# Optimization experiments

Measured on AMD Instinct MI355X. Metric: run time of the kernel, lower is better.

Reference implementation:

```python
import jax, jax.numpy as jnp
import numpy as np

N_NODES = 100000
IN_F, HID_F, OUT_F = 128, 128, 64
N_EDGES = 1600000


def _gcn_conv(x, src, dst, n, W, b):
    # x: [N, Fin]; src/dst: [E'] (self-loops already appended)
    h = x @ W                                        # [N, Fout]
    deg = jax.ops.segment_sum(jnp.ones_like(dst, dtype=h.dtype), dst,
                              num_segments=n)        # in-degree incl. self-loop
    dinv = jnp.where(deg > 0, jax.lax.rsqrt(deg), 0.0)
    norm = dinv[src] * dinv[dst]                     # [E']
    msg = h[src] * norm[:, None]                     # [E', Fout] gather + scale
    out = jax.ops.segment_sum(msg, dst, num_segments=n)
    return out + b


def setup_inputs() -> dict:
    key = jax.random.key(0)
    ks = jax.random.split(key, 6)
    x = jax.random.normal(ks[0], (N_NODES, IN_F), dtype=jnp.float32)
    edge_index = jax.random.randint(ks[1], (2, N_EDGES), 0, N_NODES, dtype=jnp.int64)
    # Glorot-ish init for weights, zeros for biases (PyG GCNConv default)
    W1 = jax.random.normal(ks[2], (IN_F, HID_F), dtype=jnp.float32) / np.sqrt(IN_F)
    b1 = jnp.zeros((HID_F,), dtype=jnp.float32)
    W2 = jax.random.normal(ks[3], (HID_F, OUT_F), dtype=jnp.float32) / np.sqrt(HID_F)
    b2 = jnp.zeros((OUT_F,), dtype=jnp.float32)
    return {"x": x, "edge_index": edge_index, "W1": W1, "b1": b1, "W2": W2, "b2": b2}


def reference(x, edge_index, W1, b1, W2, b2):
    n = x.shape[0]
    # GCNConv adds self-loops, then symmetric deg^-1/2 normalization
    loops = jnp.arange(n, dtype=edge_index.dtype)
    src = jnp.concatenate([edge_index[0], loops])
    dst = jnp.concatenate([edge_index[1], loops])
    h = _gcn_conv(x, src, dst, n, W1, b1)
    h = jax.nn.relu(h)
    out = _gcn_conv(h, src, dst, n, W2, b2)
    return out
```

## Files before the change

kernel.cpp:

```cpp
#include <hip/hip_runtime.h>
#include <hip/hip_fp16.h>

#define N_NODES 100000
#define N_EDGES 1600000
#define BNODES  128
#define NBUCK   782
#define CAP     3072
#define BIN_TILE 8192
#define BIN_BLOCKS 196
#define LDSK    136


typedef _Float16 half8 __attribute__((ext_vector_type(8)));
typedef float    f32x4 __attribute__((ext_vector_type(4)));

__device__ __forceinline__ float bcf(float v, int l) {
    return __int_as_float(__builtin_amdgcn_readlane(__float_as_int(v), l));
}
__device__ __forceinline__ int bci(int v, int l) {
    return __builtin_amdgcn_readlane(v, l);
}


__global__ __launch_bounds__(1024, 1) void k_bin(const int* __restrict__ src,
                                                 const int* __restrict__ dst,
                                                 int* __restrict__ cursor,
                                                 unsigned int* __restrict__ staged) {
    __shared__ unsigned int stg[BIN_TILE];
    __shared__ unsigned short stgb[BIN_TILE];
    __shared__ int hist[NBUCK];
    __shared__ int lbase[NBUCK];
    __shared__ int gbs[NBUCK];
    __shared__ int wsum[16];

    int t = threadIdx.x;
    int lane = t & 63, wv = t >> 6;
    long base = (long)blockIdx.x * BIN_TILE;
    int nval = (int)min((long)BIN_TILE, (long)N_EDGES - base);

    for (int i = t; i < NBUCK; i += 1024) hist[i] = 0;
    __syncthreads();

    unsigned int ent[8], brk[8];
#pragma unroll
    for (int r = 0; r < 8; r++) {
        int i = r * 1024 + t;
        if (i < nval) {
            int s = src[base + i], d = dst[base + i];
            int b = d >> 7;
            int rk = atomicAdd(&hist[b], 1);
            ent[r] = ((unsigned int)(d & 127) << 17) | (unsigned int)s;
            brk[r] = ((unsigned int)b << 16) | (unsigned int)rk;
        } else {
            brk[r] = 0xFFFFFFFFu;
        }
    }
    __syncthreads();

    {
        int v = (t < NBUCK) ? hist[t] : 0;
        int x = v;
#pragma unroll
        for (int o = 1; o < 64; o <<= 1) {
            int u = __shfl_up(x, o);
            if (lane >= o) x += u;
        }
        if (lane == 63) wsum[wv] = x;
        __syncthreads();
        if (wv == 0) {
            int ws = (lane < 16) ? wsum[lane] : 0;
#pragma unroll
            for (int o = 1; o < 16; o <<= 1) {
                int u = __shfl_up(ws, o);
                if (lane >= o) ws += u;
            }
            if (lane < 16) wsum[lane] = ws;
        }
        __syncthreads();
        int incl = x + (wv > 0 ? wsum[wv - 1] : 0);
        if (t < NBUCK) lbase[t] = incl - v;
    }
    __syncthreads();

#pragma unroll
    for (int r = 0; r < 8; r++) {
        if (brk[r] != 0xFFFFFFFFu) {
            int b  = (int)(brk[r] >> 16);
            int rk = (int)(brk[r] & 0xFFFF);
            int p  = lbase[b] + rk;
            stg[p]  = ent[r];
            stgb[p] = (unsigned short)b;
        }
    }
    __syncthreads();

    if (t < NBUCK) gbs[t] = (hist[t] > 0) ? atomicAdd(&cursor[t], hist[t]) : 0;
    __syncthreads();

    for (int i = t; i < nval; i += 1024) {
        int b = stgb[i];
        int pos = gbs[b] + (i - lbase[b]);
        if (pos < CAP) staged[(size_t)b * CAP + pos] = stg[i];
    }
}


__global__ __launch_bounds__(512) void k_fill3(const unsigned int* __restrict__ staged,
                                               const int* __restrict__ cursor,
                                               int* __restrict__ col,
                                               int2* __restrict__ rpse,
                                               float* __restrict__ dinv) {
    __shared__ int stg[CAP];
    __shared__ int lcnt[BNODES];
    __shared__ int lbase[BNODES];
    __shared__ int lpos[BNODES];
    __shared__ int sscan[BNODES];

    int b = blockIdx.x, t = threadIdx.x;
    int n = min(cursor[b], CAP);
    const unsigned int* sp = staged + (size_t)b * CAP;

    if (t < BNODES) lcnt[t] = 0;
    __syncthreads();

    unsigned int ent[CAP / 512];
#pragma unroll
    for (int r = 0; r < CAP / 512; r++) {
        int i = r * 512 + t;
        if (i < n) {
            ent[r] = sp[i];
            atomicAdd(&lcnt[ent[r] >> 17], 1);
        }
    }
    __syncthreads();

    if (t < BNODES) sscan[t] = lcnt[t];
    __syncthreads();
    for (int o = 1; o < BNODES; o <<= 1) {
        int u = (t < BNODES && t >= o) ? sscan[t - o] : 0;
        __syncthreads();
        if (t < BNODES) sscan[t] += u;
        __syncthreads();
    }
    if (t < BNODES) {
        int ex = sscan[t] - lcnt[t];
        lbase[t] = ex;
        lpos[t]  = ex;
        int node = b * BNODES + t;
        if (node < N_NODES) {
            dinv[node] = rsqrtf((float)(lcnt[t] + 1));
            rpse[node] = make_int2(b * CAP + ex, b * CAP + ex + lcnt[t]);
        }
    }
    __syncthreads();

#pragma unroll
    for (int r = 0; r < CAP / 512; r++) {
        int i = r * 512 + t;
        if (i < n) {
            int dl = (int)(ent[r] >> 17);
            int pos = atomicAdd(&lpos[dl], 1);
            stg[pos] = (int)(ent[r] & 0x1FFFFu);
        }
    }
    __syncthreads();

    for (int i = t; i < n; i += 512) col[(size_t)b * CAP + i] = stg[i];
}


template <int NOUT, bool F32IN>
__global__ __launch_bounds__(256) void k_gemm_mfma(const void* __restrict__ Xv,
                                                   const float* __restrict__ W,
                                                   __half* __restrict__ H) {
    __shared__ _Float16 wt[NOUT * LDSK];
    for (int idx = threadIdx.x; idx < 64 * NOUT; idx += 256) {
        int kp = idx / NOUT;
        int n  = idx - kp * NOUT;
        __half2 p = __floats2half2_rn(W[(2 * kp) * NOUT + n], W[(2 * kp + 1) * NOUT + n]);
        *reinterpret_cast<__half2*>(&wt[n * LDSK + 2 * kp]) = p;
    }
    __syncthreads();

    int wv = threadIdx.x >> 6, l = threadIdx.x & 63;
    int m = l & 15, g = l >> 4;
    int row0 = blockIdx.x * 64 + wv * 16;
    int lrow = min(row0 + m, N_NODES - 1);

    f32x4 acc[NOUT / 16];
#pragma unroll
    for (int c = 0; c < NOUT / 16; c++) acc[c] = (f32x4){0.f, 0.f, 0.f, 0.f};

#pragma unroll
    for (int kk = 0; kk < 4; kk++) {
        int k0 = kk * 32 + g * 8;
        half8 a;
        if (F32IN) {
            const float* xp = (const float*)Xv + (size_t)lrow * 128 + k0;
#pragma unroll
            for (int j = 0; j < 8; j++) a[j] = (_Float16)xp[j];
        } else {
            a = *reinterpret_cast<const half8*>((const _Float16*)Xv + (size_t)lrow * 128 + k0);
        }
#pragma unroll
        for (int c = 0; c < NOUT / 16; c++) {
            half8 b = *reinterpret_cast<const half8*>(&wt[(c * 16 + m) * LDSK + k0]);
            acc[c] = __builtin_amdgcn_mfma_f32_16x16x32_f16(a, b, acc[c], 0, 0, 0);
        }
    }

#pragma unroll
    for (int c = 0; c < NOUT / 16; c++)
#pragma unroll
        for (int r = 0; r < 4; r++) {
            int grow = row0 + g * 4 + r;
            if (grow < N_NODES)
                H[(size_t)grow * NOUT + c * 16 + m] = __float2half(acc[c][r]);
        }
}


__global__ __launch_bounds__(256) void k_agg1(const __half2* __restrict__ H1,
                                              const float* __restrict__ dinv,
                                              const int2* __restrict__ rpse,
                                              const int* __restrict__ col,
                                              const float* __restrict__ b1,
                                              __half2* __restrict__ H2) {
    int node = blockIdx.x * 4 + (threadIdx.x >> 6);
    int lane = threadIdx.x & 63;

    float di = dinv[node];
    int2 se = rpse[node];
    int e0 = se.x, e1 = se.y;

    float2 sv = __half22float2(H1[(size_t)node * 64 + lane]);
    float a0 = sv.x * di * di, a1 = sv.y * di * di;

    for (int cb = e0; cb < e1; cb += 64) {
        int n = min(64, e1 - cb);
        int idx = cb + lane;
        int cv = col[idx < e1 ? idx : e0];
        float wf = dinv[cv] * di;

        int j = 0;
        for (; j + 8 <= n; j += 8) {
            float2 v[8];
            float  w[8];
#pragma unroll
            for (int q = 0; q < 8; q++) {
                int s = bci(cv, j + q);
                w[q] = bcf(wf, j + q);
                v[q] = __half22float2(H1[(size_t)s * 64 + lane]);
            }
#pragma unroll
            for (int q = 0; q < 8; q++) { a0 += v[q].x * w[q]; a1 += v[q].y * w[q]; }
        }
        for (; j < n; j++) {
            int s = bci(cv, j);
            float w = bcf(wf, j);
            float2 v = __half22float2(H1[(size_t)s * 64 + lane]);
            a0 += v.x * w;
            a1 += v.y * w;
        }
    }

    a0 = fmaxf(a0 + b1[2 * lane], 0.f);
    a1 = fmaxf(a1 + b1[2 * lane + 1], 0.f);
    H2[(size_t)node * 64 + lane] = __floats2half2_rn(a0, a1);
}


__global__ __launch_bounds__(256) void k_agg2(const __half* __restrict__ H3,
                                              const float* __restrict__ dinv,
                                              const int2* __restrict__ rpse,
                                              const int* __restrict__ col,
                                              const float* __restrict__ b2,
                                              float* __restrict__ out) {
    int node = (blockIdx.x * 256 + threadIdx.x) >> 6;
    int lane = threadIdx.x & 63;
    if (node >= N_NODES) return;

    float di = dinv[node];
    int2 se = rpse[node];
    int e0 = se.x, e1 = se.y;

    float a = __half2float(H3[(size_t)node * 64 + lane]) * di * di;

    for (int cb = e0; cb < e1; cb += 64) {
        int n = min(64, e1 - cb);
        int idx = cb + lane;
        int cv = col[idx < e1 ? idx : e0];
        float wf = dinv[cv] * di;

        int j = 0;
        for (; j + 8 <= n; j += 8) {
            float hv[8];
            float w[8];
#pragma unroll
            for (int q = 0; q < 8; q++) {
                int s = bci(cv, j + q);
                w[q] = bcf(wf, j + q);
                hv[q] = __half2float(H3[(size_t)s * 64 + lane]);
            }
#pragma unroll
            for (int q = 0; q < 8; q++) a += hv[q] * w[q];
        }
        for (; j < n; j++) {
            int s = bci(cv, j);
            float w = bcf(wf, j);
            a += __half2float(H3[(size_t)s * 64 + lane]) * w;
        }
    }

    out[(size_t)node * 64 + lane] = a + b2[lane];
}


extern "C" void kernel_launch(void* const* d_in, const int* in_sizes, int n_in,
                              void* d_out, int out_size, void* d_ws, size_t ws_size,
                              hipStream_t stream) {
    const float* x  = (const float*)d_in[0];
    const int*   ei = (const int*)d_in[1];
    const float* W1 = (const float*)d_in[2];
    const float* b1 = (const float*)d_in[3];
    const float* W2 = (const float*)d_in[4];
    const float* b2 = (const float*)d_in[5];
    float* out = (float*)d_out;

    const int* src = ei;
    const int* dst = ei + N_EDGES;

    char* ws = (char*)d_ws;
    size_t off = 0;
    auto alloc = [&](size_t bytes) -> void* {
        off = (off + 255) & ~(size_t)255;
        void* p = ws + off;
        off += bytes;
        return p;
    };
    int*          cursor = (int*)alloc((size_t)NBUCK * 4);
    float*        dinv   = (float*)alloc((size_t)N_NODES * 4);
    int2*         rpse   = (int2*)alloc((size_t)N_NODES * 8);
    unsigned int* staged = (unsigned int*)alloc((size_t)NBUCK * CAP * 4);
    int*          col    = (int*)alloc((size_t)NBUCK * CAP * 4);
    __half*       h1     = (__half*)alloc((size_t)N_NODES * 128 * 2);
    __half*       h2     = (__half*)alloc((size_t)N_NODES * 128 * 2);
    __half*       h3     = (__half*)alloc((size_t)N_NODES * 64 * 2);

    hipMemsetAsync(cursor, 0, (size_t)NBUCK * 4, stream);

    k_bin<<<BIN_BLOCKS, 1024, 0, stream>>>(src, dst, cursor, staged);
    k_fill3<<<NBUCK, 512, 0, stream>>>(staged, cursor, col, rpse, dinv);

    int gblk = (N_NODES + 63) / 64;

    k_gemm_mfma<128, true><<<gblk, 256, 0, stream>>>(x, W1, h1);
    k_agg1<<<N_NODES / 4, 256, 0, stream>>>((const __half2*)h1, dinv, rpse, col, b1,
                                            (__half2*)h2);

    k_gemm_mfma<64, false><<<gblk, 256, 0, stream>>>(h2, W2, h3);
    k_agg2<<<(N_NODES * 64 + 255) / 256, 256, 0, stream>>>(h3, dinv, rpse, col, b2, out);
}
```

Measured before the change: 196.3 us.

## Widen aggregation gathers to 8-byte loads, processing multiple edges per wavefront

The aggregation kernels now have each lane load 8 bytes (four halves) per gathered row instead of 4 or 2 bytes. Layer 1 handles two edges per wavefront step and layer 2 handles four, with shuffles distributing edge indices and weights and a cross-lane xor reduction at the end. The intent is fewer, wider memory transactions and more edges in flight per wave, cutting per-edge instruction and latency overhead. In exchange it adds shuffles, padding logic for partial groups, and a final reduction; in layer 2 half the lanes sit idle during the write.

```diff
diff --git a/kernel.cpp b/kernel.cpp
--- a/kernel.cpp
+++ b/kernel.cpp
@@ -16,9 +16,6 @@
 
 __device__ __forceinline__ float bcf(float v, int l) {
     return __int_as_float(__builtin_amdgcn_readlane(__float_as_int(v), l));
-}
-__device__ __forceinline__ int bci(int v, int l) {
-    return __builtin_amdgcn_readlane(v, l);
 }
 
 
@@ -220,7 +217,7 @@
 }
 
 
-__global__ __launch_bounds__(256) void k_agg1(const __half2* __restrict__ H1,
+__global__ __launch_bounds__(256) void k_agg1(const _Float16* __restrict__ H1,
                                               const float* __restrict__ dinv,
                                               const int2* __restrict__ rpse,
                                               const int* __restrict__ col,
@@ -228,13 +225,13 @@
                                               __half2* __restrict__ H2) {
     int node = blockIdx.x * 4 + (threadIdx.x >> 6);
     int lane = threadIdx.x & 63;
+    int k = lane & 31, h = lane >> 5;
 
     float di = dinv[node];
     int2 se = rpse[node];
     int e0 = se.x, e1 = se.y;
 
-    float2 sv = __half22float2(H1[(size_t)node * 64 + lane]);
-    float a0 = sv.x * di * di, a1 = sv.y * di * di;
+    float a0 = 0.f, a1 = 0.f, a2 = 0.f, a3 = 0.f;
 
     for (int cb = e0; cb < e1; cb += 64) {
         int n = min(64, e1 - cb);
@@ -242,35 +239,52 @@
         int cv = col[idx < e1 ? idx : e0];
         float wf = dinv[cv] * di;
 
-        int j = 0;
-        for (; j + 8 <= n; j += 8) {
+        for (int j = 0; j < n; j += 16) {
             float2 v[8];
             float  w[8];
 #pragma unroll
             for (int q = 0; q < 8; q++) {
-                int s = bci(cv, j + q);
-                w[q] = bcf(wf, j + q);
-                v[q] = __half22float2(H1[(size_t)s * 64 + lane]);
+                if (j + 2 * q < n) {
+                    int e  = j + 2 * q + h;
+                    int es = e < n ? e : (n - 1);
+                    int   s  = __shfl(cv, es);
+                    float ww = __shfl(wf, es);
+                    w[q] = (e < n) ? ww : 0.f;
+                    v[q] = reinterpret_cast<const float2*>(H1 + (size_t)s * 128)[k];
+                } else {
+                    w[q] = 0.f;
+                    v[q] = make_float2(0.f, 0.f);
+                }
             }
 #pragma unroll
-            for (int q = 0; q < 8; q++) { a0 += v[q].x * w[q]; a1 += v[q].y * w[q]; }
-        }
-        for (; j < n; j++) {
-            int s = bci(cv, j);
-            float w = bcf(wf, j);
-            float2 v = __half22float2(H1[(size_t)s * 64 + lane]);
-            a0 += v.x * w;
-            a1 += v.y * w;
-        }
-    }
-
-    a0 = fmaxf(a0 + b1[2 * lane], 0.f);
-    a1 = fmaxf(a1 + b1[2 * lane + 1], 0.f);
-    H2[(size_t)node * 64 + lane] = __floats2half2_rn(a0, a1);
-}
-
-
-__global__ __launch_bounds__(256) void k_agg2(const __half* __restrict__ H3,
+            for (int q = 0; q < 8; q++) {
+                __half2 pa = *reinterpret_cast<__half2*>(&v[q].x);
+                __half2 pb = *reinterpret_cast<__half2*>(&v[q].y);
+                float2 fa = __half22float2(pa), fb = __half22float2(pb);
+                a0 += fa.x * w[q];
+                a1 += fa.y * w[q];
+                a2 += fb.x * w[q];
+                a3 += fb.y * w[q];
+            }
+        }
+    }
+
+    a0 += __shfl_xor(a0, 32);
+    a1 += __shfl_xor(a1, 32);
+    a2 += __shfl_xor(a2, 32);
+    a3 += __shfl_xor(a3, 32);
+
+    float s0 = h ? a2 : a0;
+    float s1 = h ? a3 : a1;
+    const __half2* H1v = reinterpret_cast<const __half2*>(H1);
+    float2 sv = __half22float2(H1v[(size_t)node * 64 + 2 * k + h]);
+    s0 = fmaxf(s0 + sv.x * di * di + b1[4 * k + 2 * h], 0.f);
+    s1 = fmaxf(s1 + sv.y * di * di + b1[4 * k + 2 * h + 1], 0.f);
+    H2[(size_t)node * 64 + 2 * k + h] = __floats2half2_rn(s0, s1);
+}
+
+
+__global__ __launch_bounds__(256) void k_agg2(const _Float16* __restrict__ H3,
                                               const float* __restrict__ dinv,
                                               const int2* __restrict__ rpse,
                                               const int* __restrict__ col,
@@ -279,12 +293,13 @@
     int node = (blockIdx.x * 256 + threadIdx.x) >> 6;
     int lane = threadIdx.x & 63;
     if (node >= N_NODES) return;
+    int k = lane & 15, q4 = lane >> 4;
 
     float di = dinv[node];
     int2 se = rpse[node];
     int e0 = se.x, e1 = se.y;
 
-    float a = __half2float(H3[(size_t)node * 64 + lane]) * di * di;
+    float a0 = 0.f, a1 = 0.f, a2 = 0.f, a3 = 0.f;
 
     for (int cb = e0; cb < e1; cb += 64) {
         int n = min(64, e1 - cb);
@@ -292,27 +307,52 @@
         int cv = col[idx < e1 ? idx : e0];
         float wf = dinv[cv] * di;
 
-        int j = 0;
-        for (; j + 8 <= n; j += 8) {
-            float hv[8];
-            float w[8];
+        for (int j = 0; j < n; j += 32) {
+            float2 v[8];
+            float  w[8];
 #pragma unroll
             for (int q = 0; q < 8; q++) {
-                int s = bci(cv, j + q);
-                w[q] = bcf(wf, j + q);
-                hv[q] = __half2float(H3[(size_t)s * 64 + lane]);
+                if (j + 4 * q < n) {
+                    int e  = j + 4 * q + q4;
+                    int es = e < n ? e : (n - 1);
+                    int   s  = __shfl(cv, es);
+                    float ww = __shfl(wf, es);
+                    w[q] = (e < n) ? ww : 0.f;
+                    v[q] = reinterpret_cast<const float2*>(H3 + (size_t)s * 64)[k];
+                } else {
+                    w[q] = 0.f;
+                    v[q] = make_float2(0.f, 0.f);
+                }
             }
 #pragma unroll
-            for (int q = 0; q < 8; q++) a += hv[q] * w[q];
-        }
-        for (; j < n; j++) {
-            int s = bci(cv, j);
-            float w = bcf(wf, j);
-            a += __half2float(H3[(size_t)s * 64 + lane]) * w;
-        }
-    }
-
-    out[(size_t)node * 64 + lane] = a + b2[lane];
+            for (int q = 0; q < 8; q++) {
+                __half2 pa = *reinterpret_cast<__half2*>(&v[q].x);
+                __half2 pb = *reinterpret_cast<__half2*>(&v[q].y);
+                float2 fa = __half22float2(pa), fb = __half22float2(pb);
+                a0 += fa.x * w[q];
+                a1 += fa.y * w[q];
+                a2 += fb.x * w[q];
+                a3 += fb.y * w[q];
+            }
+        }
+    }
+
+    a0 += __shfl_xor(a0, 16); a1 += __shfl_xor(a1, 16);
+    a2 += __shfl_xor(a2, 16); a3 += __shfl_xor(a3, 16);
+    a0 += __shfl_xor(a0, 32); a1 += __shfl_xor(a1, 32);
+    a2 += __shfl_xor(a2, 32); a3 += __shfl_xor(a3, 32);
+
+    if (lane < 32) {
+        int hh = lane >> 4;
+        float s0 = hh ? a2 : a0;
+        float s1 = hh ? a3 : a1;
+        const __half2* H3v = reinterpret_cast<const __half2*>(H3);
+        float2 sv = __half22float2(H3v[(size_t)node * 32 + 2 * k + hh]);
+        s0 += sv.x * di * di + b2[4 * k + 2 * hh];
+        s1 += sv.y * di * di + b2[4 * k + 2 * hh + 1];
+        float2 r{s0, s1};
+        *reinterpret_cast<float2*>(out + (size_t)node * 64 + 4 * k + 2 * hh) = r;
+    }
 }
 
 
@@ -343,9 +383,9 @@
     int2*         rpse   = (int2*)alloc((size_t)N_NODES * 8);
     unsigned int* staged = (unsigned int*)alloc((size_t)NBUCK * CAP * 4);
     int*          col    = (int*)alloc((size_t)NBUCK * CAP * 4);
-    __half*       h1     = (__half*)alloc((size_t)N_NODES * 128 * 2);
-    __half*       h2     = (__half*)alloc((size_t)N_NODES * 128 * 2);
-    __half*       h3     = (__half*)alloc((size_t)N_NODES * 64 * 2);
+    _Float16*     h1     = (_Float16*)alloc((size_t)N_NODES * 128 * 2);
+    _Float16*     h2     = (_Float16*)alloc((size_t)N_NODES * 128 * 2);
+    _Float16*     h3     = (_Float16*)alloc((size_t)N_NODES * 64 * 2);
 
     hipMemsetAsync(cursor, 0, (size_t)NBUCK * 4, stream);
 
@@ -354,10 +394,9 @@
 
     int gblk = (N_NODES + 63) / 64;
 
-    k_gemm_mfma<128, true><<<gblk, 256, 0, stream>>>(x, W1, h1);
-    k_agg1<<<N_NODES / 4, 256, 0, stream>>>((const __half2*)h1, dinv, rpse, col, b1,
-                                            (__half2*)h2);
-
-    k_gemm_mfma<64, false><<<gblk, 256, 0, stream>>>(h2, W2, h3);
+    k_gemm_mfma<128, true><<<gblk, 256, 0, stream>>>(x, W1, (__half*)h1);
+    k_agg1<<<N_NODES / 4, 256, 0, stream>>>(h1, dinv, rpse, col, b1, (__half2*)h2);
+
+    k_gemm_mfma<64, false><<<gblk, 256, 0, stream>>>(h2, W2, (__half*)h3);
     k_agg2<<<(N_NODES * 64 + 255) / 256, 256, 0, stream>>>(h3, dinv, rpse, col, b2, out);
 }
```

Result: faster. 181.6 us (-7.5%).
